# Kernel optimization log

Measured on AMD Instinct MI355X. Metric: run time of the kernel, lower is better.

Reference implementation:

```python
import jax, jax.numpy as jnp
import numpy as np

DIM = 640
M_SPATIAL = 100  # 10*10
BATCH = 64
EPS = 1e-5


def setup_inputs() -> dict:
    key = jax.random.key(0)
    kx, = jax.random.split(key, 1)
    x = jax.random.normal(kx, (BATCH, DIM, M_SPATIAL), dtype=jnp.float32)
    # temperature buffer: log(1 / (2 * H * W)) as in BDC.__init__
    t = jnp.log(1.0 / (2.0 * M_SPATIAL) * jnp.ones((1, 1), dtype=jnp.float32))
    return {"x": x, "t": t}


def reference(x, t):
    B, dim, M = x.shape
    # x_pow2 = x @ x^T  -> [B, dim, dim]
    x_pow2 = jnp.einsum('bim,bjm->bij', x, x)
    # I_M.bmm(x_pow2*I) broadcasts diag along rows; (x_pow2*I).bmm(I_M) along cols
    d = jnp.diagonal(x_pow2, axis1=1, axis2=2)  # [B, dim], squared norms
    dcov = d[:, :, None] + d[:, None, :] - 2.0 * x_pow2
    dcov = jnp.clip(dcov, 0.0)
    dcov = jnp.exp(t) * dcov
    dcov = jnp.sqrt(dcov + EPS)
    # double centering: dcov.bmm(I_M) = row sums broadcast, I_M.bmm(dcov) = col sums
    row_mean = jnp.sum(dcov, axis=2, keepdims=True) / dim          # [B, dim, 1]
    col_mean = jnp.sum(dcov, axis=1, keepdims=True) / dim          # [B, 1, dim]
    grand_mean = jnp.sum(dcov, axis=(1, 2), keepdims=True) / (dim * dim)
    bdc = dcov - row_mean - col_mean + grand_mean                   # [B, dim, dim]
    # Triuvec: upper triangle incl. diagonal, row-major order
    iu_r, iu_c = np.triu_indices(dim)
    return bdc[:, iu_r, iu_c]  # [B, dim*(dim+1)//2]
```

## Files before the change

kernel.cpp:

```cpp
#include <hip/hip_runtime.h>
#include <math.h>

#define BATCH 64
#define DIM   640
#define MSP   100
#define BT    128
#define NT2   5
#define NPAIR2 15
#define NBLK2 960
#define WT    32
#define NTW   20
#define NPAIRW 210
#define NPADW  212
#define NBLKW  3392
#define PTRI  205120
#define EPSV  1e-5f

#define WS_D 0
#define WS_S 40960
#define WS_G 81920
#define XB_OFF 327936ull

typedef __attribute__((ext_vector_type(8))) short short8;
typedef __attribute__((ext_vector_type(4))) float f32x4;

__device__ __forceinline__ short f2bf(float f) {
    union { float f; unsigned u; } x; x.f = f;
    unsigned r = x.u + 0x7fffu + ((x.u >> 16) & 1u);
    return (short)(r >> 16);
}
__device__ __forceinline__ float bf2f(short h) {
    union { unsigned u; float f; } x; x.u = ((unsigned)(unsigned short)h) << 16;
    return x.f;
}

template <int NT_>
__device__ __forceinline__ void decode_pairN(int u, int& ti, int& tj) {
    ti = 0;
    while (u >= NT_ - ti) { u -= NT_ - ti; ++ti; }
    tj = ti + u;
}

__device__ __forceinline__ void decode_block128(int bid, int& b, int& ti, int& tj) {
    const int xcd = bid & 7;
    const int idx = bid >> 3;
    b = xcd + 8 * (idx & 7);
    decode_pairN<NT2>(idx >> 3, ti, tj);
}

__global__ __launch_bounds__(256) void k_prep(const float* __restrict__ x,
                                              float* __restrict__ ws) {
    short* xb = (short*)((char*)ws + XB_OFF);
    const int t = threadIdx.x;
    const int rr = t >> 4, c = t & 15;
    const int row = blockIdx.x * 16 + rr;
    const int k0 = c * 8;
    const float* src = x + (size_t)row * MSP;

    float v[8];
#pragma unroll
    for (int e = 0; e < 8; ++e) v[e] = 0.f;
    if (k0 <= 88) {
        float4 u0 = *(const float4*)(src + k0);
        float4 u1 = *(const float4*)(src + k0 + 4);
        v[0] = u0.x; v[1] = u0.y; v[2] = u0.z; v[3] = u0.w;
        v[4] = u1.x; v[5] = u1.y; v[6] = u1.z; v[7] = u1.w;
    } else if (k0 == 96) {
        float4 u0 = *(const float4*)(src + 96);
        v[0] = u0.x; v[1] = u0.y; v[2] = u0.z; v[3] = u0.w;
    }

    short8 h; float s = 0.f;
#pragma unroll
    for (int e = 0; e < 8; ++e) {
        short hb = f2bf(v[e]);
        float vr = bf2f(hb);
        s += vr * vr;
        h[e] = hb;
    }
    *(short8*)(xb + (size_t)blockIdx.x * 2048 + c * 128 + rr * 8) = h;

    s += __shfl_xor(s, 1); s += __shfl_xor(s, 2);
    s += __shfl_xor(s, 4); s += __shfl_xor(s, 8);
    if (c == 0) { ws[WS_D + row] = s; ws[WS_S + row] = 0.f; }
    if (blockIdx.x == 0 && t < BATCH) ws[WS_G + t] = 0.f;
}

__global__ __launch_bounds__(256) void k_sums(const float* __restrict__ tsc,
                                              float* __restrict__ ws) {
    __shared__ float sRow[BT];
    __shared__ float sCol[BT];

    int b, ti, tj;
    decode_block128(blockIdx.x, b, ti, tj);
    const int i0 = ti * BT, j0 = tj * BT;
    const int tid = threadIdx.x;
    const short* xb = (const short*)((const char*)ws + XB_OFF);

    if (tid < BT) { sRow[tid] = 0.f; sCol[tid] = 0.f; }

    const int wave = tid >> 6, lane = tid & 63;
    const int lm = lane & 15, lq = lane >> 4;
    const int r0 = (wave >> 1) * 64, c0 = (wave & 1) * 64;

    const short* pa = xb + (size_t)(b * 40 + ((i0 + r0) >> 4)) * 2048 + lq * 128 + lm * 8;
    const short* pb = xb + (size_t)(b * 40 + ((j0 + c0) >> 4)) * 2048 + lq * 128 + lm * 8;

    f32x4 acc[4][4] = {};
#pragma unroll
    for (int ks = 0; ks < 4; ++ks) {
        short8 af[4], bf[4];
#pragma unroll
        for (int m = 0; m < 4; ++m) af[m] = *(const short8*)(pa + m * 2048 + ks * 512);
#pragma unroll
        for (int n = 0; n < 4; ++n) bf[n] = *(const short8*)(pb + n * 2048 + ks * 512);
#pragma unroll
        for (int m = 0; m < 4; ++m)
#pragma unroll
            for (int n = 0; n < 4; ++n)
                acc[m][n] = __builtin_amdgcn_mfma_f32_16x16x32_bf16(af[m], bf[n], acc[m][n], 0, 0, 0);
    }

    const float scale = expf(tsc[0]);
    const float* dn = ws + WS_D + b * DIM;
    float dj[4];
#pragma unroll
    for (int n = 0; n < 4; ++n) dj[n] = dn[j0 + c0 + 16 * n + lm];

    float rp[4][4] = {}, cp[4] = {};
#pragma unroll
    for (int m = 0; m < 4; ++m) {
        float di_[4];
#pragma unroll
        for (int r = 0; r < 4; ++r) di_[r] = dn[i0 + r0 + 16 * m + 4 * lq + r];
#pragma unroll
        for (int n = 0; n < 4; ++n)
#pragma unroll
            for (int p = 0; p < 4; ++p) {
                float v = __builtin_amdgcn_sqrtf(
                    fmaf(scale, fmaxf(fmaf(-2.f, acc[m][n][p], di_[p] + dj[n]), 0.f), EPSV));
                rp[m][p] += v; cp[n] += v;
            }
    }

    __syncthreads();
#pragma unroll
    for (int m = 0; m < 4; ++m)
#pragma unroll
        for (int p = 0; p < 4; ++p) {
            float v = rp[m][p];
            v += __shfl_xor(v, 1); v += __shfl_xor(v, 2);
            v += __shfl_xor(v, 4); v += __shfl_xor(v, 8);
            if (lm == 0) atomicAdd(&sRow[r0 + 16 * m + 4 * lq + p], v);
        }
#pragma unroll
    for (int n = 0; n < 4; ++n) {
        float v = cp[n];
        v += __shfl_xor(v, 16); v += __shfl_xor(v, 32);
        if (lq == 0) atomicAdd(&sCol[c0 + 16 * n + lm], v);
    }
    __syncthreads();

    float* S = ws + WS_S + b * DIM;
    if (tid < BT) {
        atomicAdd(&S[i0 + tid], sRow[tid]);
        if (ti != tj) atomicAdd(&S[j0 + tid], sCol[tid]);
        float gg = sRow[tid];
        gg += __shfl_xor(gg, 1);  gg += __shfl_xor(gg, 2);  gg += __shfl_xor(gg, 4);
        gg += __shfl_xor(gg, 8);  gg += __shfl_xor(gg, 16); gg += __shfl_xor(gg, 32);
        if (lane == 0) atomicAdd(&ws[WS_G + b], (ti == tj ? 1.f : 2.f) * gg);
    }
}

__global__ __launch_bounds__(256) void k_write(const float* __restrict__ tsc,
                                               const float* __restrict__ ws,
                                               float* __restrict__ out) {
    const int tid = threadIdx.x;
    const int wave = tid >> 6, lane = tid & 63;
    const int lm = lane & 15, lq = lane >> 4;

    const int bid = blockIdx.x;
    const int xcd = bid & 7;
    const int idx = bid >> 3;
    const int b = xcd + 8 * (idx & 7);
    const int pr = (idx >> 3) * 4 + wave;
    if (pr >= NPAIRW) return;
    int ti, tj;
    decode_pairN<NTW>(pr, ti, tj);
    const int i0 = ti * WT, j0 = tj * WT;

    const short* xb = (const short*)((const char*)ws + XB_OFF);
    const short* pa = xb + (size_t)(b * 40 + 2 * ti) * 2048 + lq * 128 + lm * 8;
    const short* pb = xb + (size_t)(b * 40 + 2 * tj) * 2048 + lq * 128 + lm * 8;

    f32x4 acc[2][2] = {};
#pragma unroll
    for (int ks = 0; ks < 4; ++ks) {
        short8 a0 = *(const short8*)(pa + ks * 512);
        short8 a1 = *(const short8*)(pa + 2048 + ks * 512);
        short8 b0 = *(const short8*)(pb + ks * 512);
        short8 b1 = *(const short8*)(pb + 2048 + ks * 512);
        acc[0][0] = __builtin_amdgcn_mfma_f32_16x16x32_bf16(a0, b0, acc[0][0], 0, 0, 0);
        acc[0][1] = __builtin_amdgcn_mfma_f32_16x16x32_bf16(a0, b1, acc[0][1], 0, 0, 0);
        acc[1][0] = __builtin_amdgcn_mfma_f32_16x16x32_bf16(a1, b0, acc[1][0], 0, 0, 0);
        acc[1][1] = __builtin_amdgcn_mfma_f32_16x16x32_bf16(a1, b1, acc[1][1], 0, 0, 0);
    }

    const float scale = expf(tsc[0]);
    const float inv = 1.f / (float)DIM;
    const float g = ws[WS_G + b] * (inv * inv);
    const float* S  = ws + WS_S + b * DIM;
    const float* dn = ws + WS_D + b * DIM;

    const bool pred = (ti == tj);
    float di[2][4], ai[2][4]; int ib[2][4];
#pragma unroll
    for (int m = 0; m < 2; ++m)
#pragma unroll
        for (int r = 0; r < 4; ++r) {
            int i = i0 + 16 * m + 4 * lq + r;
            di[m][r] = dn[i];
            ai[m][r] = g - S[i] * inv;
            ib[m][r] = i * DIM - (i * (i - 1)) / 2 - i;
        }
    float dj[2], bj[2]; int jj[2];
#pragma unroll
    for (int n = 0; n < 2; ++n) {
        int j = j0 + 16 * n + lm;
        jj[n] = j; dj[n] = dn[j]; bj[n] = -S[j] * inv;
    }

    float* outb = out + (size_t)b * PTRI;
#pragma unroll
    for (int m = 0; m < 2; ++m) {
        const int ibase = i0 + 16 * m + 4 * lq;
#pragma unroll
        for (int n = 0; n < 2; ++n)
#pragma unroll
            for (int p = 0; p < 2; ++p) {
                const int r = 2 * p;
                float d0 = di[m][r]     + dj[n];
                float d1 = di[m][r + 1] + dj[n];
                float v0 = __builtin_amdgcn_sqrtf(
                    fmaf(scale, fmaxf(fmaf(-2.f, acc[m][n][r],     d0), 0.f), EPSV));
                float v1 = __builtin_amdgcn_sqrtf(
                    fmaf(scale, fmaxf(fmaf(-2.f, acc[m][n][r + 1], d1), 0.f), EPSV));
                if (!pred || jj[n] >= ibase + r)
                    outb[ib[m][r]     + jj[n]] = v0 + ai[m][r]     + bj[n];
                if (!pred || jj[n] >= ibase + r + 1)
                    outb[ib[m][r + 1] + jj[n]] = v1 + ai[m][r + 1] + bj[n];
            }
    }
}

extern "C" void kernel_launch(void* const* d_in, const int* in_sizes, int n_in,
                              void* d_out, int out_size, void* d_ws, size_t ws_size,
                              hipStream_t stream) {
    const float* x = (const float*)d_in[0];
    const float* t = (const float*)d_in[1];
    float* out = (float*)d_out;
    float* ws  = (float*)d_ws;

    k_prep <<<dim3(BATCH * DIM / 16), 256, 0, stream>>>(x, ws);
    k_sums <<<dim3(NBLK2),            256, 0, stream>>>(t, ws);
    k_write<<<dim3(NBLKW),            256, 0, stream>>>(t, ws, out);
}
```

Before: 114.5 us.

## Fuse bf16 prep into Gram-sum kernel and replace atomics with partial-sum buffers

Removes the separate k_prep launch. k_sums now reads fp32 x directly, converts it to bf16 fragments in registers, and computes squared norms with shuffles. The diagonal blocks export the bf16 tiles and norms for k_write to reuse. Global atomic accumulation of row sums and grand sums is replaced by per-tile partial buffers, which k_write reduces itself, so no zeroing pass is needed. In exchange, each block redundantly converts fp32 inputs and k_write does extra partial-sum loads.

```diff
diff --git a/kernel.cpp b/kernel.cpp
--- a/kernel.cpp
+++ b/kernel.cpp
@@ -11,15 +11,14 @@
 #define WT    32
 #define NTW   20
 #define NPAIRW 210
-#define NPADW  212
 #define NBLKW  3392
 #define PTRI  205120
 #define EPSV  1e-5f
 
-#define WS_D 0
-#define WS_S 40960
-#define WS_G 81920
-#define XB_OFF 327936ull
+#define WS_D  0
+#define WS_SP 40960
+#define WS_GP 245760
+#define XB_OFF 987136ull
 
 typedef __attribute__((ext_vector_type(8))) short short8;
 typedef __attribute__((ext_vector_type(4))) float f32x4;
@@ -41,79 +40,80 @@
     tj = ti + u;
 }
 
-__device__ __forceinline__ void decode_block128(int bid, int& b, int& ti, int& tj) {
+__device__ __forceinline__ void decode_block128(int bid, int& b, int& u,
+                                                int& ti, int& tj) {
     const int xcd = bid & 7;
     const int idx = bid >> 3;
     b = xcd + 8 * (idx & 7);
-    decode_pairN<NT2>(idx >> 3, ti, tj);
-}
-
-__global__ __launch_bounds__(256) void k_prep(const float* __restrict__ x,
-                                              float* __restrict__ ws) {
-    short* xb = (short*)((char*)ws + XB_OFF);
-    const int t = threadIdx.x;
-    const int rr = t >> 4, c = t & 15;
-    const int row = blockIdx.x * 16 + rr;
-    const int k0 = c * 8;
-    const float* src = x + (size_t)row * MSP;
-
+    u = idx >> 3;
+    decode_pairN<NT2>(u, ti, tj);
+}
+
+__device__ __forceinline__ short8 make_frag(const float* __restrict__ xrow,
+                                            int ks, int lq, float& nacc) {
     float v[8];
 #pragma unroll
     for (int e = 0; e < 8; ++e) v[e] = 0.f;
-    if (k0 <= 88) {
-        float4 u0 = *(const float4*)(src + k0);
-        float4 u1 = *(const float4*)(src + k0 + 4);
+    if (ks < 3) {
+        const float* s = xrow + ks * 32 + lq * 8;
+        float4 u0 = *(const float4*)(s);
+        float4 u1 = *(const float4*)(s + 4);
         v[0] = u0.x; v[1] = u0.y; v[2] = u0.z; v[3] = u0.w;
         v[4] = u1.x; v[5] = u1.y; v[6] = u1.z; v[7] = u1.w;
-    } else if (k0 == 96) {
-        float4 u0 = *(const float4*)(src + 96);
+    } else if (lq == 0) {
+        float4 u0 = *(const float4*)(xrow + 96);
         v[0] = u0.x; v[1] = u0.y; v[2] = u0.z; v[3] = u0.w;
     }
-
-    short8 h; float s = 0.f;
+    short8 h;
 #pragma unroll
     for (int e = 0; e < 8; ++e) {
         short hb = f2bf(v[e]);
         float vr = bf2f(hb);
-        s += vr * vr;
+        nacc += vr * vr;
         h[e] = hb;
     }
-    *(short8*)(xb + (size_t)blockIdx.x * 2048 + c * 128 + rr * 8) = h;
-
-    s += __shfl_xor(s, 1); s += __shfl_xor(s, 2);
-    s += __shfl_xor(s, 4); s += __shfl_xor(s, 8);
-    if (c == 0) { ws[WS_D + row] = s; ws[WS_S + row] = 0.f; }
-    if (blockIdx.x == 0 && t < BATCH) ws[WS_G + t] = 0.f;
-}
-
-__global__ __launch_bounds__(256) void k_sums(const float* __restrict__ tsc,
+    return h;
+}
+
+__global__ __launch_bounds__(256) void k_sums(const float* __restrict__ x,
+                                              const float* __restrict__ tsc,
                                               float* __restrict__ ws) {
     __shared__ float sRow[BT];
     __shared__ float sCol[BT];
 
-    int b, ti, tj;
-    decode_block128(blockIdx.x, b, ti, tj);
+    int b, u, ti, tj;
+    decode_block128(blockIdx.x, b, u, ti, tj);
     const int i0 = ti * BT, j0 = tj * BT;
     const int tid = threadIdx.x;
-    const short* xb = (const short*)((const char*)ws + XB_OFF);
+    short* xbg = (short*)((char*)ws + XB_OFF);
 
     if (tid < BT) { sRow[tid] = 0.f; sCol[tid] = 0.f; }
 
     const int wave = tid >> 6, lane = tid & 63;
     const int lm = lane & 15, lq = lane >> 4;
     const int r0 = (wave >> 1) * 64, c0 = (wave & 1) * 64;
-
-    const short* pa = xb + (size_t)(b * 40 + ((i0 + r0) >> 4)) * 2048 + lq * 128 + lm * 8;
-    const short* pb = xb + (size_t)(b * 40 + ((j0 + c0) >> 4)) * 2048 + lq * 128 + lm * 8;
+    const int ra = i0 + r0, rb = j0 + c0;
+    const bool diag = (ti == tj);
+    const bool expw = diag && ((wave & 1) == 0);
+
+    const float* xba = x + ((size_t)b * DIM + ra + lm) * MSP;
+    const float* xbb = x + ((size_t)b * DIM + rb + lm) * MSP;
 
     f32x4 acc[4][4] = {};
+    float na[4] = {}, nb[4] = {};
 #pragma unroll
     for (int ks = 0; ks < 4; ++ks) {
         short8 af[4], bf[4];
 #pragma unroll
-        for (int m = 0; m < 4; ++m) af[m] = *(const short8*)(pa + m * 2048 + ks * 512);
-#pragma unroll
-        for (int n = 0; n < 4; ++n) bf[n] = *(const short8*)(pb + n * 2048 + ks * 512);
+        for (int m = 0; m < 4; ++m) {
+            af[m] = make_frag(xba + (size_t)(16 * m) * MSP, ks, lq, na[m]);
+            if (expw)
+                *(short8*)(xbg + (size_t)(b * 40 + ((ra >> 4) + m)) * 2048
+                           + (ks * 4 + lq) * 128 + lm * 8) = af[m];
+        }
+#pragma unroll
+        for (int n = 0; n < 4; ++n)
+            bf[n] = make_frag(xbb + (size_t)(16 * n) * MSP, ks, lq, nb[n]);
 #pragma unroll
         for (int m = 0; m < 4; ++m)
 #pragma unroll
@@ -121,26 +121,33 @@
                 acc[m][n] = __builtin_amdgcn_mfma_f32_16x16x32_bf16(af[m], bf[n], acc[m][n], 0, 0, 0);
     }
 
+#pragma unroll
+    for (int m = 0; m < 4; ++m) {
+        na[m] += __shfl_xor(na[m], 16); na[m] += __shfl_xor(na[m], 32);
+        nb[m] += __shfl_xor(nb[m], 16); nb[m] += __shfl_xor(nb[m], 32);
+    }
+    if (expw && lq == 0) {
+#pragma unroll
+        for (int m = 0; m < 4; ++m) ws[WS_D + b * DIM + ra + 16 * m + lm] = na[m];
+    }
+
     const float scale = expf(tsc[0]);
-    const float* dn = ws + WS_D + b * DIM;
-    float dj[4];
-#pragma unroll
-    for (int n = 0; n < 4; ++n) dj[n] = dn[j0 + c0 + 16 * n + lm];
-
     float rp[4][4] = {}, cp[4] = {};
 #pragma unroll
     for (int m = 0; m < 4; ++m) {
         float di_[4];
 #pragma unroll
-        for (int r = 0; r < 4; ++r) di_[r] = dn[i0 + r0 + 16 * m + 4 * lq + r];
-#pragma unroll
-        for (int n = 0; n < 4; ++n)
+        for (int r = 0; r < 4; ++r) di_[r] = __shfl(na[m], 4 * lq + r);
+#pragma unroll
+        for (int n = 0; n < 4; ++n) {
+            const float djn = nb[n];
 #pragma unroll
             for (int p = 0; p < 4; ++p) {
                 float v = __builtin_amdgcn_sqrtf(
-                    fmaf(scale, fmaxf(fmaf(-2.f, acc[m][n][p], di_[p] + dj[n]), 0.f), EPSV));
+                    fmaf(scale, fmaxf(fmaf(-2.f, acc[m][n][p], di_[p] + djn), 0.f), EPSV));
                 rp[m][p] += v; cp[n] += v;
             }
+        }
     }
 
     __syncthreads();
@@ -161,14 +168,17 @@
     }
     __syncthreads();
 
-    float* S = ws + WS_S + b * DIM;
+    float* sp = ws + WS_SP;
     if (tid < BT) {
-        atomicAdd(&S[i0 + tid], sRow[tid]);
-        if (ti != tj) atomicAdd(&S[j0 + tid], sCol[tid]);
-        float gg = sRow[tid];
+        sp[((b * 5 + ti) * 5 + tj) * 128 + tid] = sRow[tid];
+        if (!diag)
+            sp[((b * 5 + tj) * 5 + ti) * 128 + tid] = sCol[tid];
+    }
+    if (tid < 64) {
+        float gg = sRow[tid] + sRow[tid + 64];
         gg += __shfl_xor(gg, 1);  gg += __shfl_xor(gg, 2);  gg += __shfl_xor(gg, 4);
         gg += __shfl_xor(gg, 8);  gg += __shfl_xor(gg, 16); gg += __shfl_xor(gg, 32);
-        if (lane == 0) atomicAdd(&ws[WS_G + b], (ti == tj ? 1.f : 2.f) * gg);
+        if (tid == 0) ws[WS_GP + b * 15 + u] = (diag ? 1.f : 2.f) * gg;
     }
 }
 
@@ -189,6 +199,17 @@
     decode_pairN<NTW>(pr, ti, tj);
     const int i0 = ti * WT, j0 = tj * WT;
 
+    float Sv;
+    {
+        const int ix = (lane < 32) ? (i0 + lane) : (j0 + (lane - 32));
+        const float* p = ws + WS_SP + (size_t)((b * 5 + (ix >> 7)) * 5) * 128
+                         + (ix & 127);
+        Sv = p[0] + p[128] + p[256] + p[384] + p[512];
+    }
+    float gv = (lane < 15) ? ws[WS_GP + b * 15 + lane] : 0.f;
+    gv += __shfl_xor(gv, 1);  gv += __shfl_xor(gv, 2);  gv += __shfl_xor(gv, 4);
+    gv += __shfl_xor(gv, 8);  gv += __shfl_xor(gv, 16); gv += __shfl_xor(gv, 32);
+
     const short* xb = (const short*)((const char*)ws + XB_OFF);
     const short* pa = xb + (size_t)(b * 40 + 2 * ti) * 2048 + lq * 128 + lm * 8;
     const short* pb = xb + (size_t)(b * 40 + 2 * tj) * 2048 + lq * 128 + lm * 8;
@@ -208,8 +229,7 @@
 
     const float scale = expf(tsc[0]);
     const float inv = 1.f / (float)DIM;
-    const float g = ws[WS_G + b] * (inv * inv);
-    const float* S  = ws + WS_S + b * DIM;
+    const float g = gv * (inv * inv);
     const float* dn = ws + WS_D + b * DIM;
 
     const bool pred = (ti == tj);
@@ -220,14 +240,15 @@
         for (int r = 0; r < 4; ++r) {
             int i = i0 + 16 * m + 4 * lq + r;
             di[m][r] = dn[i];
-            ai[m][r] = g - S[i] * inv;
+            ai[m][r] = g - __shfl(Sv, 16 * m + 4 * lq + r) * inv;
             ib[m][r] = i * DIM - (i * (i - 1)) / 2 - i;
         }
     float dj[2], bj[2]; int jj[2];
 #pragma unroll
     for (int n = 0; n < 2; ++n) {
         int j = j0 + 16 * n + lm;
-        jj[n] = j; dj[n] = dn[j]; bj[n] = -S[j] * inv;
+        jj[n] = j; dj[n] = dn[j];
+        bj[n] = -__shfl(Sv, 32 + 16 * n + lm) * inv;
     }
 
     float* outb = out + (size_t)b * PTRI;
@@ -261,7 +282,6 @@
     float* out = (float*)d_out;
     float* ws  = (float*)d_ws;
 
-    k_prep <<<dim3(BATCH * DIM / 16), 256, 0, stream>>>(x, ws);
-    k_sums <<<dim3(NBLK2),            256, 0, stream>>>(t, ws);
-    k_write<<<dim3(NBLKW),            256, 0, stream>>>(t, ws, out);
-}
+    k_sums <<<dim3(NBLK2), 256, 0, stream>>>(x, t, ws);
+    k_write<<<dim3(NBLKW), 256, 0, stream>>>(t, ws, out);
+}
```

Result: slower. 136.0 us (+18.8%).
